# Kernel optimization log

Measured on AMD Instinct MI355X. Metric: run time of the kernel, lower is better.

The kernel has to match this reference:

```python
import jax, jax.numpy as jnp
import numpy as np

B, N_OBJ, FEAT_IN = 512, 3, 2048
FEAT_SIZE = 512
EMBED = 512
HID = 512
VOCAB = 4096
MAX_LEN = 40
T = MAX_LEN - 2  # sampled steps between SOS and appended EOS
SOS_IDX, EOS_IDX = 1, 2
TAU = 1.0


def setup_inputs() -> dict:
    key = jax.random.key(0)
    ks = jax.random.split(key, 16)
    s = lambda k, shape, fan: jax.random.normal(k, shape, jnp.float32) / np.sqrt(fan)
    feats = jax.random.normal(ks[0], (B, N_OBJ, FEAT_IN), jnp.float32)
    targets = jax.random.randint(ks[1], (B,), 0, N_OBJ)
    feat_W = s(ks[2], (FEAT_SIZE, FEAT_IN), FEAT_IN)
    feat_b = jnp.zeros((FEAT_SIZE,), jnp.float32)
    emb_W = s(ks[3], (VOCAB, EMBED), EMBED)
    init_W = s(ks[4], (HID, N_OBJ * (FEAT_SIZE + 1)), N_OBJ * (FEAT_SIZE + 1))
    init_b = jnp.zeros((HID,), jnp.float32)
    gru_Wih = s(ks[5], (3 * HID, EMBED), EMBED)
    gru_Whh = s(ks[6], (3 * HID, HID), HID)
    gru_bih = jnp.zeros((3 * HID,), jnp.float32)
    gru_bhh = jnp.zeros((3 * HID,), jnp.float32)
    out_W = s(ks[7], (VOCAB, HID), HID)
    out_b = jnp.zeros((VOCAB,), jnp.float32)
    # pre-sampled gumbel noise for the T decode steps
    u = jax.random.uniform(ks[8], (T, B, VOCAB), jnp.float32, 1e-10, 1.0)
    gumbel = -jnp.log(-jnp.log(u))
    return dict(feats=feats, targets=targets, feat_W=feat_W, feat_b=feat_b,
                emb_W=emb_W, init_W=init_W, init_b=init_b,
                gru_Wih=gru_Wih, gru_Whh=gru_Whh, gru_bih=gru_bih,
                gru_bhh=gru_bhh, out_W=out_W, out_b=out_b, gumbel=gumbel)


def _gru_cell(x, h, Wih, Whh, bih, bhh):
    gi = x @ Wih.T + bih              # [B, 3H]
    gh = h @ Whh.T + bhh
    i_r, i_z, i_n = jnp.split(gi, 3, axis=-1)
    h_r, h_z, h_n = jnp.split(gh, 3, axis=-1)
    r = jax.nn.sigmoid(i_r + h_r)
    z = jax.nn.sigmoid(i_z + h_z)
    n = jnp.tanh(i_n + r * h_n)
    return (1.0 - z) * n + z * h


def _decode(feats, targets, feat_W, feat_b, emb_W, init_W, init_b,
            gru_Wih, gru_Whh, gru_bih, gru_bhh, out_W, out_b, gumbel):
    bsz = feats.shape[0]
    # embed_features: linear feat model per object + target one-hot
    fe = jnp.einsum('boi,hi->boh', feats, feat_W) + feat_b      # [B,3,F]
    t_oh = jax.nn.one_hot(targets, N_OBJ, dtype=feats.dtype)    # [B,3]
    ft = jnp.concatenate([fe, t_oh[:, :, None]], axis=2).reshape(bsz, -1)
    h0 = ft @ init_W.T + init_b                                  # [B,H]

    sos_oh = jax.nn.one_hot(jnp.full((bsz,), SOS_IDX), VOCAB, dtype=feats.dtype)
    x0 = sos_oh @ emb_W                                          # [B,E]
    done0 = jnp.zeros((bsz,), bool)
    len0 = jnp.ones((bsz,), jnp.int32)                           # counts SOS

    def step(carry, g):
        h, x, done, length = carry
        h = _gru_cell(x, h, gru_Wih, gru_Whh, gru_bih, gru_bhh)
        logits = h @ out_W.T + out_b                             # [B,V]
        soft = jax.nn.softmax((logits + g) / TAU, axis=-1)
        pred = jnp.argmax(soft, axis=-1)
        hard = jax.nn.one_hot(pred, VOCAB, dtype=soft.dtype)
        oh = hard + soft - jax.lax.stop_gradient(soft)           # straight-through
        length = length + (~done).astype(jnp.int32)
        done = done | (pred == EOS_IDX)
        x = oh @ emb_W
        return (h, x, done, length), oh

    (_, _, done, length), ohs = jax.lax.scan(step, (h0, x0, done0, len0), gumbel)
    length = length + (~done).astype(jnp.int32)                  # appended EOS

    eos_oh = jax.nn.one_hot(jnp.full((bsz,), EOS_IDX), VOCAB, dtype=feats.dtype)
    lang = jnp.concatenate(
        [sos_oh[:, None], jnp.transpose(ohs, (1, 0, 2)), eos_oh[:, None]], axis=1)
    mask = (jnp.arange(MAX_LEN)[None, :] < length[:, None])      # zero past length
    lang = lang * mask[:, :, None].astype(lang.dtype)
    return lang, length


def reference(feats, targets, feat_W, feat_b, emb_W, init_W, init_b,
              gru_Wih, gru_Whh, gru_bih, gru_bhh, out_W, out_b, gumbel):
    lang, length = _decode(feats, targets, feat_W, feat_b, emb_W, init_W, init_b,
                           gru_Wih, gru_Whh, gru_bih, gru_bhh, out_W, out_b, gumbel)
    eos_loss = jnp.float32(0.0)
    return lang, length, eos_loss
```

## Files before the change

kernel.cpp:

```cpp
#include <hip/hip_runtime.h>
#include <cstdint>
#include <cstddef>

#define BATCH   512
#define HIDDEN  512
#define EMB     512
#define VOCAB   4096
#define NOBJ    3
#define FEATIN  2048
#define FEATSZ  512
#define MAXLEN  40
#define TSTEPS  38
#define SOS     1
#define EOS     2
#define GIH     1536
#define KCH     256

#define BK 16
#define BM 64

#define NLOGITS_BLK 512
#define NGATES_BLK  384
#define NCOMB_BLK   (NLOGITS_BLK + NGATES_BLK)

static __device__ __forceinline__ unsigned long long pack_key(float v, int col) {
    uint32_t u = __float_as_uint(v);
    u = (u & 0x80000000u) ? ~u : (u | 0x80000000u);
    return ((unsigned long long)u << 32) | (uint32_t)(VOCAB - 1 - col);
}

__global__ __launch_bounds__(256) void k_zero(float* __restrict__ out, int n,
                                              unsigned long long* __restrict__ keys) {
    int tid = threadIdx.x;
    size_t base = (size_t)blockIdx.x * 4096;
#pragma unroll
    for (int s = 0; s < 4; ++s) {
        size_t i4 = base + (size_t)s * 1024 + (size_t)tid * 4;
        if (i4 + 3 < (size_t)n) {
            *(float4*)&out[i4] = make_float4(0.f, 0.f, 0.f, 0.f);
        } else {
            for (size_t j = i4; j < (size_t)n; ++j) out[j] = 0.f;
        }
    }
    size_t gi = (size_t)blockIdx.x * 256 + tid;
    if (gi < (size_t)TSTEPS * BATCH) keys[gi] = 0ULL;
}

__global__ __launch_bounds__(256) void k_fe(const float* __restrict__ feats,
                                            const float* __restrict__ featW,
                                            const float* __restrict__ featb,
                                            float* __restrict__ fe) {
    __shared__ float As[BK][BM];
    __shared__ float Bs[BK][BM];
    const int tid = threadIdx.x;
    const int m0 = blockIdx.y * BM, n0 = blockIdx.x * BM;
    const int tx = tid & 15, ty = tid >> 4;
    const int lrow = tid >> 2, lk = (tid & 3) << 2;
    float acc[4][4] = {};
    for (int k0 = 0; k0 < FEATIN; k0 += BK) {
        float4 a = *(const float4*)&feats[(size_t)(m0 + lrow) * FEATIN + k0 + lk];
        float4 b = *(const float4*)&featW[(size_t)(n0 + lrow) * FEATIN + k0 + lk];
        __syncthreads();
        As[lk+0][lrow] = a.x; As[lk+1][lrow] = a.y; As[lk+2][lrow] = a.z; As[lk+3][lrow] = a.w;
        Bs[lk+0][lrow] = b.x; Bs[lk+1][lrow] = b.y; Bs[lk+2][lrow] = b.z; Bs[lk+3][lrow] = b.w;
        __syncthreads();
#pragma unroll
        for (int kk = 0; kk < BK; ++kk) {
            float4 av = *(const float4*)&As[kk][ty * 4];
            float4 bv = *(const float4*)&Bs[kk][tx * 4];
            float ar[4] = {av.x, av.y, av.z, av.w};
            float br[4] = {bv.x, bv.y, bv.z, bv.w};
#pragma unroll
            for (int i = 0; i < 4; ++i)
#pragma unroll
                for (int j = 0; j < 4; ++j) acc[i][j] += ar[i] * br[j];
        }
    }
#pragma unroll
    for (int i = 0; i < 4; ++i) {
        int r = m0 + ty * 4 + i;
#pragma unroll
        for (int j = 0; j < 4; ++j) {
            int c = n0 + tx * 4 + j;
            fe[(size_t)r * FEATSZ + c] = acc[i][j] + featb[c];
        }
    }
}

__global__ __launch_bounds__(256) void k_h0(const float* __restrict__ fe,
                                            const float* __restrict__ initW,
                                            const float* __restrict__ initb,
                                            const int* __restrict__ targets,
                                            float* __restrict__ h) {
    __shared__ float As[BK][BM];
    __shared__ float Bs[BK][BM];
    const int tid = threadIdx.x;
    const int m0 = blockIdx.y * BM, n0 = blockIdx.x * BM;
    const int tx = tid & 15, ty = tid >> 4;
    const int lrow = tid >> 2, lk = (tid & 3) << 2;
    float acc[4][4] = {};
    const int K = NOBJ * FEATSZ;
    for (int k0 = 0; k0 < K; k0 += BK) {
        float4 a = *(const float4*)&fe[(size_t)(m0 + lrow) * K + k0 + lk];
        float breg[4];
#pragma unroll
        for (int i = 0; i < 4; ++i) {
            int ka = k0 + lk + i;
            breg[i] = initW[(size_t)(n0 + lrow) * 1539 + ka + (ka >> 9)];
        }
        __syncthreads();
        As[lk+0][lrow] = a.x; As[lk+1][lrow] = a.y; As[lk+2][lrow] = a.z; As[lk+3][lrow] = a.w;
#pragma unroll
        for (int i = 0; i < 4; ++i) Bs[lk + i][lrow] = breg[i];
        __syncthreads();
#pragma unroll
        for (int kk = 0; kk < BK; ++kk) {
            float4 av = *(const float4*)&As[kk][ty * 4];
            float4 bv = *(const float4*)&Bs[kk][tx * 4];
            float ar[4] = {av.x, av.y, av.z, av.w};
            float br[4] = {bv.x, bv.y, bv.z, bv.w};
#pragma unroll
            for (int i = 0; i < 4; ++i)
#pragma unroll
                for (int j = 0; j < 4; ++j) acc[i][j] += ar[i] * br[j];
        }
    }
#pragma unroll
    for (int i = 0; i < 4; ++i) {
        int r = m0 + ty * 4 + i;
        int tg = targets[r];
#pragma unroll
        for (int j = 0; j < 4; ++j) {
            int c = n0 + tx * 4 + j;
            h[(size_t)r * HIDDEN + c] =
                acc[i][j] + initb[c] + initW[(size_t)c * 1539 + tg * 513 + 512];
        }
    }
}

__global__ __launch_bounds__(256) void k_P(const float* __restrict__ embW,
                                           const float* __restrict__ Wih,
                                           const float* __restrict__ bih,
                                           float* __restrict__ P) {
    __shared__ __align__(16) float As[2][BK][BM + 4];
    __shared__ __align__(16) float Bs[2][BK][128 + 4];
    const int tid = threadIdx.x;
    const int arow = tid >> 2, ak = (tid & 3) << 2;
    const int tx = tid & 15, ty = tid >> 4;
    const int m0 = blockIdx.y * BM, n0 = blockIdx.x * 128;
    const float* Ap = embW + (size_t)(m0 + arow) * EMB;
    const float* Bp0 = Wih + (size_t)(n0 + arow) * EMB;
    const float* Bp1 = Wih + (size_t)(n0 + 64 + arow) * EMB;
    float4 aR = *(const float4*)&Ap[ak];
    float4 bR0 = *(const float4*)&Bp0[ak];
    float4 bR1 = *(const float4*)&Bp1[ak];
    float acc[4][8] = {};
    int buf = 0;
    for (int k0 = 0; k0 < EMB; k0 += BK) {
        As[buf][ak+0][arow] = aR.x; As[buf][ak+1][arow] = aR.y;
        As[buf][ak+2][arow] = aR.z; As[buf][ak+3][arow] = aR.w;
        Bs[buf][ak+0][arow] = bR0.x; Bs[buf][ak+1][arow] = bR0.y;
        Bs[buf][ak+2][arow] = bR0.z; Bs[buf][ak+3][arow] = bR0.w;
        Bs[buf][ak+0][arow+64] = bR1.x; Bs[buf][ak+1][arow+64] = bR1.y;
        Bs[buf][ak+2][arow+64] = bR1.z; Bs[buf][ak+3][arow+64] = bR1.w;
        __syncthreads();
        if (k0 + BK < EMB) {
            aR  = *(const float4*)&Ap[k0 + BK + ak];
            bR0 = *(const float4*)&Bp0[k0 + BK + ak];
            bR1 = *(const float4*)&Bp1[k0 + BK + ak];
        }
#pragma unroll
        for (int kk = 0; kk < BK; ++kk) {
            float4 av  = *(const float4*)&As[buf][kk][ty * 4];
            float4 bv0 = *(const float4*)&Bs[buf][kk][tx * 4];
            float4 bv1 = *(const float4*)&Bs[buf][kk][64 + tx * 4];
            float ar[4] = {av.x, av.y, av.z, av.w};
            float br[8] = {bv0.x, bv0.y, bv0.z, bv0.w, bv1.x, bv1.y, bv1.z, bv1.w};
#pragma unroll
            for (int i = 0; i < 4; ++i)
#pragma unroll
                for (int j = 0; j < 8; ++j) acc[i][j] += ar[i] * br[j];
        }
        buf ^= 1;
    }
    float4 bi0 = *(const float4*)&bih[n0 + tx * 4];
    float4 bi1 = *(const float4*)&bih[n0 + 64 + tx * 4];
#pragma unroll
    for (int i = 0; i < 4; ++i) {
        int r = m0 + ty * 4 + i;
        *(float4*)&P[(size_t)r * GIH + n0 + tx * 4] =
            make_float4(acc[i][0] + bi0.x, acc[i][1] + bi0.y, acc[i][2] + bi0.z, acc[i][3] + bi0.w);
        *(float4*)&P[(size_t)r * GIH + n0 + 64 + tx * 4] =
            make_float4(acc[i][4] + bi1.x, acc[i][5] + bi1.y, acc[i][6] + bi1.z, acc[i][7] + bi1.w);
    }
}

__global__ __launch_bounds__(256) void k_comb(const float* __restrict__ h,
                                              const float* __restrict__ Whh,
                                              float* __restrict__ Gp,
                                              const float* __restrict__ outW,
                                              const float* __restrict__ outb,
                                              const float* __restrict__ gum_t,
                                              unsigned long long* __restrict__ keys_t,
                                              int do_logits, int do_gates) {
    __shared__ __align__(16) float As[2][BK][BM + 4];
    __shared__ __align__(16) float Bs[2][BK][BM + 4];
    __shared__ unsigned long long red[BM][16];
    const int tid = threadIdx.x;
    const int arow = tid >> 2, ak = (tid & 3) << 2;
    const int tx = tid & 15, ty = tid >> 4;
    const int bx = blockIdx.x;

    if (bx < NLOGITS_BLK) {
        if (!do_logits) return;
        const int n0 = (bx & 63) * 64, m0 = (bx >> 6) * 64;
        const float* Ap = h + (size_t)(m0 + arow) * HIDDEN;
        const float* Bp = outW + (size_t)(n0 + arow) * HIDDEN;
        float4 aR = *(const float4*)&Ap[ak];
        float4 bR = *(const float4*)&Bp[ak];
        float acc[4][4] = {};
        int buf = 0;
        for (int k0 = 0; k0 < HIDDEN; k0 += BK) {
            As[buf][ak+0][arow] = aR.x; As[buf][ak+1][arow] = aR.y;
            As[buf][ak+2][arow] = aR.z; As[buf][ak+3][arow] = aR.w;
            Bs[buf][ak+0][arow] = bR.x; Bs[buf][ak+1][arow] = bR.y;
            Bs[buf][ak+2][arow] = bR.z; Bs[buf][ak+3][arow] = bR.w;
            __syncthreads();
            if (k0 + BK < HIDDEN) {
                aR = *(const float4*)&Ap[k0 + BK + ak];
                bR = *(const float4*)&Bp[k0 + BK + ak];
            }
#pragma unroll
            for (int kk = 0; kk < BK; ++kk) {
                float4 av = *(const float4*)&As[buf][kk][ty * 4];
                float4 bv = *(const float4*)&Bs[buf][kk][tx * 4];
                float ar[4] = {av.x, av.y, av.z, av.w};
                float br[4] = {bv.x, bv.y, bv.z, bv.w};
#pragma unroll
                for (int i = 0; i < 4; ++i)
#pragma unroll
                    for (int j = 0; j < 4; ++j) acc[i][j] += ar[i] * br[j];
            }
            buf ^= 1;
        }
        float4 ob = *(const float4*)&outb[n0 + tx * 4];
        float obr[4] = {ob.x, ob.y, ob.z, ob.w};
#pragma unroll
        for (int i = 0; i < 4; ++i) {
            int r = m0 + ty * 4 + i;
            float4 g = *(const float4*)&gum_t[(size_t)r * VOCAB + n0 + tx * 4];
            float gr[4] = {g.x, g.y, g.z, g.w};
            unsigned long long best = 0ULL;
#pragma unroll
            for (int j = 0; j < 4; ++j) {
                int c = n0 + tx * 4 + j;
                unsigned long long key = pack_key(acc[i][j] + obr[j] + gr[j], c);
                if (key > best) best = key;
            }
            red[ty * 4 + i][tx] = best;
        }
        __syncthreads();
        if (tid < BM) {
            unsigned long long best = red[tid][0];
#pragma unroll
            for (int q = 1; q < 16; ++q)
                if (red[tid][q] > best) best = red[tid][q];
            atomicMax(&keys_t[m0 + tid], best);
        }
    } else {
        if (!do_gates) return;
        const int gx = bx - NLOGITS_BLK;
        const int jn = gx % 24;
        const int rest = gx / 24;
        const int jm = rest & 7, kc = rest >> 3;
        const int m0 = jm * 64, n0 = jn * 64;
        const float* Ap = h + (size_t)(m0 + arow) * HIDDEN + kc * KCH;
        const float* Bp = Whh + (size_t)(n0 + arow) * HIDDEN + kc * KCH;
        float4 aR = *(const float4*)&Ap[ak];
        float4 bR = *(const float4*)&Bp[ak];
        float acc[4][4] = {};
        int buf = 0;
        for (int k0 = 0; k0 < KCH; k0 += BK) {
            As[buf][ak+0][arow] = aR.x; As[buf][ak+1][arow] = aR.y;
            As[buf][ak+2][arow] = aR.z; As[buf][ak+3][arow] = aR.w;
            Bs[buf][ak+0][arow] = bR.x; Bs[buf][ak+1][arow] = bR.y;
            Bs[buf][ak+2][arow] = bR.z; Bs[buf][ak+3][arow] = bR.w;
            __syncthreads();
            if (k0 + BK < KCH) {
                aR = *(const float4*)&Ap[k0 + BK + ak];
                bR = *(const float4*)&Bp[k0 + BK + ak];
            }
#pragma unroll
            for (int kk = 0; kk < BK; ++kk) {
                float4 av = *(const float4*)&As[buf][kk][ty * 4];
                float4 bv = *(const float4*)&Bs[buf][kk][tx * 4];
                float ar[4] = {av.x, av.y, av.z, av.w};
                float br[4] = {bv.x, bv.y, bv.z, bv.w};
#pragma unroll
                for (int i = 0; i < 4; ++i)
#pragma unroll
                    for (int j = 0; j < 4; ++j) acc[i][j] += ar[i] * br[j];
            }
            buf ^= 1;
        }
        float* Go = Gp + (size_t)(kc * BATCH) * GIH;
#pragma unroll
        for (int i = 0; i < 4; ++i) {
            int r = m0 + ty * 4 + i;
            *(float4*)&Go[(size_t)r * GIH + n0 + tx * 4] =
                make_float4(acc[i][0], acc[i][1], acc[i][2], acc[i][3]);
        }
    }
}

__global__ __launch_bounds__(256) void k_gru(const float* __restrict__ Gp,
                                             const float* __restrict__ P,
                                             const float* __restrict__ bhh,
                                             const unsigned long long* __restrict__ keys_prev,
                                             float* __restrict__ h) {
    int idx = blockIdx.x * 256 + threadIdx.x;
    int b = idx >> 7;
    int j4 = (idx & 127) << 2;
    int tok = SOS;
    if (keys_prev) tok = (VOCAB - 1) - (int)(uint32_t)(keys_prev[b] & 0xffffffffULL);
    const float* Pr = P + (size_t)tok * GIH;
    const float* G0 = Gp + (size_t)b * GIH;
    const float* G1 = Gp + (size_t)(BATCH + b) * GIH;
    float4 ir = *(const float4*)&Pr[j4];
    float4 iz = *(const float4*)&Pr[j4 + HIDDEN];
    float4 in_ = *(const float4*)&Pr[j4 + 2 * HIDDEN];
    float4 hr0 = *(const float4*)&G0[j4];
    float4 hz0 = *(const float4*)&G0[j4 + HIDDEN];
    float4 hn0 = *(const float4*)&G0[j4 + 2 * HIDDEN];
    float4 hr1 = *(const float4*)&G1[j4];
    float4 hz1 = *(const float4*)&G1[j4 + HIDDEN];
    float4 hn1 = *(const float4*)&G1[j4 + 2 * HIDDEN];
    float4 bhr = *(const float4*)&bhh[j4];
    float4 bhz = *(const float4*)&bhh[j4 + HIDDEN];
    float4 bhn = *(const float4*)&bhh[j4 + 2 * HIDDEN];
    float4 ho = *(const float4*)&h[(size_t)b * HIDDEN + j4];
    float irr[4] = {ir.x, ir.y, ir.z, ir.w};
    float izz[4] = {iz.x, iz.y, iz.z, iz.w};
    float inn[4] = {in_.x, in_.y, in_.z, in_.w};
    float hrr[4] = {hr0.x + hr1.x + bhr.x, hr0.y + hr1.y + bhr.y,
                    hr0.z + hr1.z + bhr.z, hr0.w + hr1.w + bhr.w};
    float hzz[4] = {hz0.x + hz1.x + bhz.x, hz0.y + hz1.y + bhz.y,
                    hz0.z + hz1.z + bhz.z, hz0.w + hz1.w + bhz.w};
    float hnn[4] = {hn0.x + hn1.x + bhn.x, hn0.y + hn1.y + bhn.y,
                    hn0.z + hn1.z + bhn.z, hn0.w + hn1.w + bhn.w};
    float hov[4] = {ho.x, ho.y, ho.z, ho.w};
    float res[4];
#pragma unroll
    for (int i = 0; i < 4; ++i) {
        float r = 1.0f / (1.0f + expf(-(irr[i] + hrr[i])));
        float z = 1.0f / (1.0f + expf(-(izz[i] + hzz[i])));
        float n = tanhf(inn[i] + r * hnn[i]);
        res[i] = (1.0f - z) * n + z * hov[i];
    }
    *(float4*)&h[(size_t)b * HIDDEN + j4] = make_float4(res[0], res[1], res[2], res[3]);
}

__global__ __launch_bounds__(256) void k_final(const unsigned long long* __restrict__ keys,
                                               float* __restrict__ out) {
    int b = blockIdx.x * 256 + threadIdx.x;
    if (b >= BATCH) return;
    int toks[TSTEPS];
    int len = 1;
    bool done = false;
#pragma unroll
    for (int t = 0; t < TSTEPS; ++t) {
        int tok = (VOCAB - 1) - (int)(uint32_t)(keys[(size_t)t * BATCH + b] & 0xffffffffULL);
        toks[t] = tok;
        if (!done) len++;
        if (tok == EOS) done = true;
    }
    if (!done) len++;
    float* lang = out + (size_t)b * MAXLEN * VOCAB;
    lang[SOS] = 1.0f;
#pragma unroll
    for (int t = 0; t < TSTEPS; ++t) {
        int pos = t + 1;
        if (pos < len) lang[(size_t)pos * VOCAB + toks[t]] = 1.0f;
    }
    if (len == MAXLEN) lang[(size_t)(MAXLEN - 1) * VOCAB + EOS] = 1.0f;
    out[(size_t)BATCH * MAXLEN * VOCAB + b] = (float)len;
    if (b == 0) out[(size_t)BATCH * MAXLEN * VOCAB + BATCH] = 0.0f;
}

extern "C" void kernel_launch(void* const* d_in, const int* in_sizes, int n_in,
                              void* d_out, int out_size, void* d_ws, size_t ws_size,
                              hipStream_t stream) {
    const float* feats = (const float*)d_in[0];
    const int*   targets = (const int*)d_in[1];
    const float* featW = (const float*)d_in[2];
    const float* featb = (const float*)d_in[3];
    const float* embW  = (const float*)d_in[4];
    const float* initW = (const float*)d_in[5];
    const float* initb = (const float*)d_in[6];
    const float* Wih   = (const float*)d_in[7];
    const float* Whh   = (const float*)d_in[8];
    const float* bih   = (const float*)d_in[9];
    const float* bhh   = (const float*)d_in[10];
    const float* outW  = (const float*)d_in[11];
    const float* outb  = (const float*)d_in[12];
    const float* gumbel = (const float*)d_in[13];
    float* out = (float*)d_out;

    char* ws = (char*)d_ws;
    float* h  = (float*)(ws);
    unsigned long long* keys = (unsigned long long*)(ws + (1 << 20));
    float* Gp = (float*)(ws + 5 * (1 << 18));
    float* fe = Gp;
    float* P  = (float*)(ws + 8 * (1 << 20));

    int zb = (out_size + 4095) / 4096;
    k_zero<<<dim3(zb), 256, 0, stream>>>(out, out_size, keys);

    k_fe<<<dim3(FEATSZ / BM, (BATCH * NOBJ) / BM), 256, 0, stream>>>(feats, featW, featb, fe);
    k_h0<<<dim3(HIDDEN / BM, BATCH / BM), 256, 0, stream>>>(fe, initW, initb, targets, h);
    k_P<<<dim3(GIH / 128, VOCAB / BM), 256, 0, stream>>>(embW, Wih, bih, P);

    k_comb<<<dim3(NCOMB_BLK), 256, 0, stream>>>(h, Whh, Gp, outW, outb, gumbel, keys, 0, 1);

    for (int t = 0; t < TSTEPS; ++t) {
        const unsigned long long* kprev = (t == 0) ? nullptr : (keys + (size_t)(t - 1) * BATCH);
        k_gru<<<dim3(BATCH * HIDDEN / 4 / 256), 256, 0, stream>>>(Gp, P, bhh, kprev, h);
        k_comb<<<dim3(NCOMB_BLK), 256, 0, stream>>>(
            h, Whh, Gp, outW, outb, gumbel + (size_t)t * BATCH * VOCAB,
            keys + (size_t)t * BATCH, 1, (t < TSTEPS - 1) ? 1 : 0);
    }
    k_final<<<dim3(2), 256, 0, stream>>>(keys, out);
}
```

Before: 2.668 ms.

## Use 64-thread blocks with 8x8 register tiles and drop gate split-K

Replaces the 256-thread combined logits/gates GEMM kernel with a 64-thread kernel where each thread computes an 8x8 output tile, which raises arithmetic intensity per shared-memory load. The Whh gate GEMM no longer splits K into two halves, so the GRU kernel reads one partial buffer instead of two. Argmax reduction now uses wavefront shuffles instead of a shared-memory table, and skipped work is handled by launching fewer blocks rather than early-returning. The trade-off is far fewer threads per block, single-buffered shared memory with two barriers per K step, and higher register pressure, which may lower latency hiding.

```diff
diff --git a/kernel.cpp b/kernel.cpp
--- a/kernel.cpp
+++ b/kernel.cpp
@@ -14,14 +14,13 @@
 #define SOS     1
 #define EOS     2
 #define GIH     1536
-#define KCH     256
 
 #define BK 16
 #define BM 64
 
 #define NLOGITS_BLK 512
-#define NGATES_BLK  384
-#define NCOMB_BLK   (NLOGITS_BLK + NGATES_BLK)
+#define NGATES_BLK  192
+#define NSTEP_BLK   (NLOGITS_BLK + NGATES_BLK)
 
 static __device__ __forceinline__ unsigned long long pack_key(float v, int col) {
     uint32_t u = __float_as_uint(v);
@@ -195,120 +194,113 @@
     }
 }
 
-__global__ __launch_bounds__(256) void k_comb(const float* __restrict__ h,
-                                              const float* __restrict__ Whh,
-                                              float* __restrict__ Gp,
-                                              const float* __restrict__ outW,
-                                              const float* __restrict__ outb,
-                                              const float* __restrict__ gum_t,
-                                              unsigned long long* __restrict__ keys_t,
-                                              int do_logits, int do_gates) {
-    __shared__ __align__(16) float As[2][BK][BM + 4];
-    __shared__ __align__(16) float Bs[2][BK][BM + 4];
-    __shared__ unsigned long long red[BM][16];
+__global__ __launch_bounds__(64) void k_step(const float* __restrict__ h,
+                                             const float* __restrict__ Whh,
+                                             float* __restrict__ Gp,
+                                             const float* __restrict__ outW,
+                                             const float* __restrict__ outb,
+                                             const float* __restrict__ gum_t,
+                                             unsigned long long* __restrict__ keys_t,
+                                             int bx_off) {
+    __shared__ float As[BK][64];
+    __shared__ float Bs[BK][64];
     const int tid = threadIdx.x;
-    const int arow = tid >> 2, ak = (tid & 3) << 2;
-    const int tx = tid & 15, ty = tid >> 4;
-    const int bx = blockIdx.x;
-
-    if (bx < NLOGITS_BLK) {
-        if (!do_logits) return;
-        const int n0 = (bx & 63) * 64, m0 = (bx >> 6) * 64;
-        const float* Ap = h + (size_t)(m0 + arow) * HIDDEN;
-        const float* Bp = outW + (size_t)(n0 + arow) * HIDDEN;
-        float4 aR = *(const float4*)&Ap[ak];
-        float4 bR = *(const float4*)&Bp[ak];
-        float acc[4][4] = {};
-        int buf = 0;
-        for (int k0 = 0; k0 < HIDDEN; k0 += BK) {
-            As[buf][ak+0][arow] = aR.x; As[buf][ak+1][arow] = aR.y;
-            As[buf][ak+2][arow] = aR.z; As[buf][ak+3][arow] = aR.w;
-            Bs[buf][ak+0][arow] = bR.x; Bs[buf][ak+1][arow] = bR.y;
-            Bs[buf][ak+2][arow] = bR.z; Bs[buf][ak+3][arow] = bR.w;
-            __syncthreads();
-            if (k0 + BK < HIDDEN) {
-                aR = *(const float4*)&Ap[k0 + BK + ak];
-                bR = *(const float4*)&Bp[k0 + BK + ak];
+    const int bx = (int)blockIdx.x + bx_off;
+    const int is_logits = (bx < NLOGITS_BLK);
+    int m0, n0;
+    const float* Bp;
+    if (is_logits) {
+        m0 = (bx >> 6) * 64;
+        n0 = (bx & 63) * 64;
+        Bp = outW + (size_t)(n0 + tid) * HIDDEN;
+    } else {
+        const int gx = bx - NLOGITS_BLK;
+        m0 = (gx / 24) * 64;
+        n0 = (gx % 24) * 64;
+        Bp = Whh + (size_t)(n0 + tid) * HIDDEN;
+    }
+    const float* Ap = h + (size_t)(m0 + tid) * HIDDEN;
+    const int ty = tid >> 3, tx = tid & 7;
+
+    float4 aR[4], bR[4];
+#pragma unroll
+    for (int q = 0; q < 4; ++q) {
+        aR[q] = *(const float4*)&Ap[q * 4];
+        bR[q] = *(const float4*)&Bp[q * 4];
+    }
+    float acc[8][8] = {};
+    for (int k0 = 0; k0 < HIDDEN; k0 += BK) {
+        __syncthreads();
+#pragma unroll
+        for (int q = 0; q < 4; ++q) {
+            As[q*4+0][tid] = aR[q].x; As[q*4+1][tid] = aR[q].y;
+            As[q*4+2][tid] = aR[q].z; As[q*4+3][tid] = aR[q].w;
+            Bs[q*4+0][tid] = bR[q].x; Bs[q*4+1][tid] = bR[q].y;
+            Bs[q*4+2][tid] = bR[q].z; Bs[q*4+3][tid] = bR[q].w;
+        }
+        __syncthreads();
+        if (k0 + BK < HIDDEN) {
+#pragma unroll
+            for (int q = 0; q < 4; ++q) {
+                aR[q] = *(const float4*)&Ap[k0 + BK + q * 4];
+                bR[q] = *(const float4*)&Bp[k0 + BK + q * 4];
             }
-#pragma unroll
-            for (int kk = 0; kk < BK; ++kk) {
-                float4 av = *(const float4*)&As[buf][kk][ty * 4];
-                float4 bv = *(const float4*)&Bs[buf][kk][tx * 4];
-                float ar[4] = {av.x, av.y, av.z, av.w};
-                float br[4] = {bv.x, bv.y, bv.z, bv.w};
-#pragma unroll
-                for (int i = 0; i < 4; ++i)
-#pragma unroll
-                    for (int j = 0; j < 4; ++j) acc[i][j] += ar[i] * br[j];
+        }
+#pragma unroll
+        for (int kk = 0; kk < BK; ++kk) {
+            float4 a0 = *(const float4*)&As[kk][ty * 8];
+            float4 a1 = *(const float4*)&As[kk][ty * 8 + 4];
+            float4 b0 = *(const float4*)&Bs[kk][tx * 8];
+            float4 b1 = *(const float4*)&Bs[kk][tx * 8 + 4];
+            float ar[8] = {a0.x, a0.y, a0.z, a0.w, a1.x, a1.y, a1.z, a1.w};
+            float br[8] = {b0.x, b0.y, b0.z, b0.w, b1.x, b1.y, b1.z, b1.w};
+#pragma unroll
+            for (int i = 0; i < 8; ++i)
+#pragma unroll
+                for (int j = 0; j < 8; ++j) acc[i][j] += ar[i] * br[j];
+        }
+    }
+
+    if (is_logits) {
+        float4 ob0 = *(const float4*)&outb[n0 + tx * 8];
+        float4 ob1 = *(const float4*)&outb[n0 + tx * 8 + 4];
+        float obr[8] = {ob0.x, ob0.y, ob0.z, ob0.w, ob1.x, ob1.y, ob1.z, ob1.w};
+        unsigned long long best[8];
+#pragma unroll
+        for (int i = 0; i < 8; ++i) {
+            int r = m0 + ty * 8 + i;
+            const float* gp = &gum_t[(size_t)r * VOCAB + n0 + tx * 8];
+            float4 g0 = *(const float4*)&gp[0];
+            float4 g1 = *(const float4*)&gp[4];
+            float gv[8] = {g0.x, g0.y, g0.z, g0.w, g1.x, g1.y, g1.z, g1.w};
+            unsigned long long bb = 0ULL;
+#pragma unroll
+            for (int j = 0; j < 8; ++j) {
+                unsigned long long key = pack_key(acc[i][j] + obr[j] + gv[j], n0 + tx * 8 + j);
+                if (key > bb) bb = key;
             }
-            buf ^= 1;
-        }
-        float4 ob = *(const float4*)&outb[n0 + tx * 4];
-        float obr[4] = {ob.x, ob.y, ob.z, ob.w};
-#pragma unroll
-        for (int i = 0; i < 4; ++i) {
-            int r = m0 + ty * 4 + i;
-            float4 g = *(const float4*)&gum_t[(size_t)r * VOCAB + n0 + tx * 4];
-            float gr[4] = {g.x, g.y, g.z, g.w};
-            unsigned long long best = 0ULL;
-#pragma unroll
-            for (int j = 0; j < 4; ++j) {
-                int c = n0 + tx * 4 + j;
-                unsigned long long key = pack_key(acc[i][j] + obr[j] + gr[j], c);
-                if (key > best) best = key;
+            best[i] = bb;
+        }
+#pragma unroll
+        for (int s = 1; s < 8; s <<= 1) {
+#pragma unroll
+            for (int i = 0; i < 8; ++i) {
+                unsigned long long o = __shfl_xor(best[i], s);
+                if (o > best[i]) best[i] = o;
             }
-            red[ty * 4 + i][tx] = best;
-        }
-        __syncthreads();
-        if (tid < BM) {
-            unsigned long long best = red[tid][0];
-#pragma unroll
-            for (int q = 1; q < 16; ++q)
-                if (red[tid][q] > best) best = red[tid][q];
-            atomicMax(&keys_t[m0 + tid], best);
+        }
+        if (tx == 0) {
+#pragma unroll
+            for (int i = 0; i < 8; ++i) atomicMax(&keys_t[m0 + ty * 8 + i], best[i]);
         }
     } else {
-        if (!do_gates) return;
-        const int gx = bx - NLOGITS_BLK;
-        const int jn = gx % 24;
-        const int rest = gx / 24;
-        const int jm = rest & 7, kc = rest >> 3;
-        const int m0 = jm * 64, n0 = jn * 64;
-        const float* Ap = h + (size_t)(m0 + arow) * HIDDEN + kc * KCH;
-        const float* Bp = Whh + (size_t)(n0 + arow) * HIDDEN + kc * KCH;
-        float4 aR = *(const float4*)&Ap[ak];
-        float4 bR = *(const float4*)&Bp[ak];
-        float acc[4][4] = {};
-        int buf = 0;
-        for (int k0 = 0; k0 < KCH; k0 += BK) {
-            As[buf][ak+0][arow] = aR.x; As[buf][ak+1][arow] = aR.y;
-            As[buf][ak+2][arow] = aR.z; As[buf][ak+3][arow] = aR.w;
-            Bs[buf][ak+0][arow] = bR.x; Bs[buf][ak+1][arow] = bR.y;
-            Bs[buf][ak+2][arow] = bR.z; Bs[buf][ak+3][arow] = bR.w;
-            __syncthreads();
-            if (k0 + BK < KCH) {
-                aR = *(const float4*)&Ap[k0 + BK + ak];
-                bR = *(const float4*)&Bp[k0 + BK + ak];
-            }
-#pragma unroll
-            for (int kk = 0; kk < BK; ++kk) {
-                float4 av = *(const float4*)&As[buf][kk][ty * 4];
-                float4 bv = *(const float4*)&Bs[buf][kk][tx * 4];
-                float ar[4] = {av.x, av.y, av.z, av.w};
-                float br[4] = {bv.x, bv.y, bv.z, bv.w};
-#pragma unroll
-                for (int i = 0; i < 4; ++i)
-#pragma unroll
-                    for (int j = 0; j < 4; ++j) acc[i][j] += ar[i] * br[j];
-            }
-            buf ^= 1;
-        }
-        float* Go = Gp + (size_t)(kc * BATCH) * GIH;
-#pragma unroll
-        for (int i = 0; i < 4; ++i) {
-            int r = m0 + ty * 4 + i;
-            *(float4*)&Go[(size_t)r * GIH + n0 + tx * 4] =
+#pragma unroll
+        for (int i = 0; i < 8; ++i) {
+            int r = m0 + ty * 8 + i;
+            *(float4*)&Gp[(size_t)r * GIH + n0 + tx * 8] =
                 make_float4(acc[i][0], acc[i][1], acc[i][2], acc[i][3]);
+            *(float4*)&Gp[(size_t)r * GIH + n0 + tx * 8 + 4] =
+                make_float4(acc[i][4], acc[i][5], acc[i][6], acc[i][7]);
         }
     }
 }
@@ -325,16 +317,12 @@
     if (keys_prev) tok = (VOCAB - 1) - (int)(uint32_t)(keys_prev[b] & 0xffffffffULL);
     const float* Pr = P + (size_t)tok * GIH;
     const float* G0 = Gp + (size_t)b * GIH;
-    const float* G1 = Gp + (size_t)(BATCH + b) * GIH;
     float4 ir = *(const float4*)&Pr[j4];
     float4 iz = *(const float4*)&Pr[j4 + HIDDEN];
     float4 in_ = *(const float4*)&Pr[j4 + 2 * HIDDEN];
     float4 hr0 = *(const float4*)&G0[j4];
     float4 hz0 = *(const float4*)&G0[j4 + HIDDEN];
     float4 hn0 = *(const float4*)&G0[j4 + 2 * HIDDEN];
-    float4 hr1 = *(const float4*)&G1[j4];
-    float4 hz1 = *(const float4*)&G1[j4 + HIDDEN];
-    float4 hn1 = *(const float4*)&G1[j4 + 2 * HIDDEN];
     float4 bhr = *(const float4*)&bhh[j4];
     float4 bhz = *(const float4*)&bhh[j4 + HIDDEN];
     float4 bhn = *(const float4*)&bhh[j4 + 2 * HIDDEN];
@@ -342,12 +330,9 @@
     float irr[4] = {ir.x, ir.y, ir.z, ir.w};
     float izz[4] = {iz.x, iz.y, iz.z, iz.w};
     float inn[4] = {in_.x, in_.y, in_.z, in_.w};
-    float hrr[4] = {hr0.x + hr1.x + bhr.x, hr0.y + hr1.y + bhr.y,
-                    hr0.z + hr1.z + bhr.z, hr0.w + hr1.w + bhr.w};
-    float hzz[4] = {hz0.x + hz1.x + bhz.x, hz0.y + hz1.y + bhz.y,
-                    hz0.z + hz1.z + bhz.z, hz0.w + hz1.w + bhz.w};
-    float hnn[4] = {hn0.x + hn1.x + bhn.x, hn0.y + hn1.y + bhn.y,
-                    hn0.z + hn1.z + bhn.z, hn0.w + hn1.w + bhn.w};
+    float hrr[4] = {hr0.x + bhr.x, hr0.y + bhr.y, hr0.z + bhr.z, hr0.w + bhr.w};
+    float hzz[4] = {hz0.x + bhz.x, hz0.y + bhz.y, hz0.z + bhz.z, hz0.w + bhz.w};
+    float hnn[4] = {hn0.x + bhn.x, hn0.y + bhn.y, hn0.z + bhn.z, hn0.w + bhn.w};
     float hov[4] = {ho.x, ho.y, ho.z, ho.w};
     float res[4];
 #pragma unroll
@@ -420,14 +405,16 @@
     k_h0<<<dim3(HIDDEN / BM, BATCH / BM), 256, 0, stream>>>(fe, initW, initb, targets, h);
     k_P<<<dim3(GIH / 128, VOCAB / BM), 256, 0, stream>>>(embW, Wih, bih, P);
 
-    k_comb<<<dim3(NCOMB_BLK), 256, 0, stream>>>(h, Whh, Gp, outW, outb, gumbel, keys, 0, 1);
+    k_step<<<dim3(NGATES_BLK), 64, 0, stream>>>(h, Whh, Gp, outW, outb, gumbel, keys,
+                                                NLOGITS_BLK);
 
     for (int t = 0; t < TSTEPS; ++t) {
         const unsigned long long* kprev = (t == 0) ? nullptr : (keys + (size_t)(t - 1) * BATCH);
         k_gru<<<dim3(BATCH * HIDDEN / 4 / 256), 256, 0, stream>>>(Gp, P, bhh, kprev, h);
-        k_comb<<<dim3(NCOMB_BLK), 256, 0, stream>>>(
+        int nblk = (t < TSTEPS - 1) ? NSTEP_BLK : NLOGITS_BLK;
+        k_step<<<dim3(nblk), 64, 0, stream>>>(
             h, Whh, Gp, outW, outb, gumbel + (size_t)t * BATCH * VOCAB,
-            keys + (size_t)t * BATCH, 1, (t < TSTEPS - 1) ? 1 : 0);
+            keys + (size_t)t * BATCH, 0);
     }
     k_final<<<dim3(2), 256, 0, stream>>>(keys, out);
 }
```

Result: slower. 3.460 ms (+29.7%).
